# Performance work log

Measured on AMD Instinct MI355X. Metric: run time of the kernel, lower is better.

Reference implementation:

```python
import jax, jax.numpy as jnp
import numpy as np

B, S, D = 512, 500, 128
NQ, NC, NQD, NCD = 10000, 500, 100, 100

def _glorot(key, shape):
    fan_in, fan_out = shape[0], shape[1]
    lim = np.sqrt(6.0 / (fan_in + fan_out))
    return jax.random.uniform(key, shape, jnp.float32, -lim, lim)

def setup_inputs() -> dict:
    key = jax.random.key(0)
    ks = jax.random.split(key, 24)
    inp = {
        'question_seq': jax.random.randint(ks[0], (B, S), 0, NQ),
        'concept_seq': jax.random.randint(ks[1], (B, S), 0, NC),
        'question_diff_seq': jax.random.randint(ks[2], (B, S), 0, NQD),
        'concept_diff_seq': jax.random.randint(ks[3], (B, S), 0, NCD),
        'correct_seq': jax.random.randint(ks[4], (B, S), 0, 2),
        # embedding tables
        'Eq': jax.random.normal(ks[5], (NQ, D), jnp.float32),
        'Ec': jax.random.normal(ks[6], (NC, D), jnp.float32),
        'Eqd': jax.random.normal(ks[7], (NQD, D), jnp.float32),
        'Ecd': jax.random.normal(ks[8], (NCD, D), jnp.float32),
        'Ecorr': jax.random.normal(ks[9], (2, D), jnp.float32),
        # linear layers (stored as [in, out], y = x @ W + b)
        'Wx': _glorot(ks[10], (4 * D, D)), 'bx': jnp.zeros((D,), jnp.float32),
        'Wsdf1': _glorot(ks[11], (D, D)), 'bsdf1': jnp.zeros((D,), jnp.float32),
        'Wsdf2': _glorot(ks[12], (D, D)), 'bsdf2': jnp.zeros((D,), jnp.float32),
        'Wpka1': _glorot(ks[13], (2 * D, D)), 'bpka1': jnp.zeros((D,), jnp.float32),
        'Wpka2': _glorot(ks[14], (2 * D, D)), 'bpka2': jnp.zeros((D,), jnp.float32),
        'Wki': _glorot(ks[15], (4 * D, D)), 'bki': jnp.zeros((D,), jnp.float32),
        # xavier_uniform init of h_pre (torch nn.init.xavier_uniform_ on zeros(B, D))
        'h0': _glorot(ks[16], (B, D)),
    }
    return inp

def reference(question_seq, concept_seq, question_diff_seq, concept_diff_seq,
              correct_seq, Eq, Ec, Eqd, Ecd, Ecorr, Wx, bx,
              Wsdf1, bsdf1, Wsdf2, bsdf2, Wpka1, bpka1, Wpka2, bpka2,
              Wki, bki, h0):
    # embed all sequences: [B, S, D]
    qe = Eq[question_seq]
    ce = Ec[concept_seq]
    qde = Eqd[question_diff_seq]
    cde = Ecd[concept_diff_seq]
    co = Ecorr[correct_seq]
    # x_t = generate_x_MLP(concat(...)) precomputed for all timesteps
    x_all = jnp.concatenate([qe, ce, qde, cde], axis=-1) @ Wx + bx  # [B, S, D]

    # time-major slices for scan over t = 0 .. S-2
    tm = lambda a: jnp.swapaxes(a, 0, 1)  # [S, B, D]
    xs = (tm(x_all)[:-1], tm(x_all)[1:], tm(co)[:-1], tm(qde)[:-1], tm(cde)[:-1])

    def step(h_pre, inputs):
        x_t, x_next, co_t, qd_t, cd_t = inputs
        input_sdf = x_t - h_pre
        sdf = jax.nn.sigmoid(input_sdf @ Wsdf1 + bsdf1) * jnp.tanh(input_sdf @ Wsdf2 + bsdf2)
        input_pka = jnp.concatenate([sdf, co_t], axis=-1)
        pka = jax.nn.sigmoid(input_pka @ Wpka1 + bpka1) * jnp.tanh(input_pka @ Wpka2 + bpka2)
        input_ki = jnp.concatenate([h_pre, co_t, qd_t, cd_t], axis=-1)
        gamma = jax.nn.sigmoid(input_ki @ Wki + bki)
        h = gamma * h_pre + (1.0 - gamma) * pka
        y_t = jax.nn.sigmoid(jnp.sum(x_next * h, axis=-1))  # [B]
        return h, y_t

    _, ys = jax.lax.scan(step, h0, xs)  # ys: [S-1, B]
    # y[:, S-1] is never written in the original (stays 0)
    y = jnp.concatenate([ys.T, jnp.zeros((question_seq.shape[0], 1), jnp.float32)], axis=1)
    return y
```

## Files before the change

### kernel.cpp

```cpp
#include <hip/hip_runtime.h>
#include <hip/hip_bf16.h>
#include <cstdint>
#include <cstddef>

#define BB 512
#define SS 500
#define TT 499
#define NRB 256
#define L2E 1.4426950408889634f

typedef float  f32x4  __attribute__((ext_vector_type(4)));
typedef short  bf16x8 __attribute__((ext_vector_type(8)));

#define MFMA16(A, B, C) __builtin_amdgcn_mfma_f32_16x16x32_bf16((A), (B), (C), 0, 0, 0)

static constexpr size_t OFF_TQ    = 0;
static constexpr size_t OFF_TC    = 10240000;
static constexpr size_t OFF_TQD   = 10752000;
static constexpr size_t OFF_TCD   = 10854400;
static constexpr size_t OFF_TCOK  = 10956800;
static constexpr size_t OFF_TP1   = 10957824;
static constexpr size_t OFF_TP2   = 10958848;
static constexpr size_t OFF_TMPA  = 10959872;
static constexpr size_t OFF_TMPB  = 11011072;
static constexpr size_t OFF_WFRAG = 11062272;
static constexpr size_t TOTAL_WS  = 11226112;

__device__ unsigned char g_fb[TOTAL_WS];

__device__ __forceinline__ unsigned short f2bf(float f) {
    union { float f; uint32_t u; } v; v.f = f;
    uint32_t u = v.u;
    uint32_t r = u + 0x7FFFu + ((u >> 16) & 1u);
    return (unsigned short)(r >> 16);
}
__device__ __forceinline__ float fsig(float z) {
    return __builtin_amdgcn_rcpf(1.0f + __expf(-z));
}
__device__ __forceinline__ uint32_t cvtpk(float lo, float hi) {
    uint32_t r;
    asm("v_cvt_pk_bf16_f32 %0, %1, %2" : "=v"(r) : "v"(lo), "v"(hi));
    return r;
}
__device__ __forceinline__ void bar_lgkm() {
    asm volatile("s_waitcnt lgkmcnt(0)" ::: "memory");
    __builtin_amdgcn_s_barrier();
}
__device__ __forceinline__ float sum16(float x) {
    int a = __float_as_int(x);
    int b = __builtin_amdgcn_update_dpp(a, a, 0xB1, 0xF, 0xF, false);
    float s = x + __int_as_float(b);
    int c = __float_as_int(s);
    int d = __builtin_amdgcn_update_dpp(c, c, 0x4E, 0xF, 0xF, false);
    s += __int_as_float(d);
    int e = __float_as_int(s);
    int f = __builtin_amdgcn_update_dpp(e, e, 0x141, 0xF, 0xF, false);
    s += __int_as_float(f);
    int gg = __float_as_int(s);
    int hh = __builtin_amdgcn_update_dpp(gg, gg, 0x140, 0xF, 0xF, false);
    return s + __int_as_float(hh);
}

__global__ __launch_bounds__(128) void k_tables(
    const float* __restrict__ Eq, const float* __restrict__ Ec,
    const float* __restrict__ Eqd, const float* __restrict__ Ecd,
    const float* __restrict__ Ecorr,
    const float* __restrict__ Wx,  const float* __restrict__ bx,
    const float* __restrict__ Wpka1, const float* __restrict__ bpka1,
    const float* __restrict__ Wpka2, const float* __restrict__ bpka2,
    const float* __restrict__ Wki, const float* __restrict__ bki,
    float* __restrict__ TQ, float* __restrict__ TC,
    float* __restrict__ TQD, float* __restrict__ TCD,
    float* __restrict__ TCOk, float* __restrict__ Tp1, float* __restrict__ Tp2,
    float* __restrict__ tmpA, float* __restrict__ tmpB)
{
    int blk = blockIdx.x;
    const float* A; const float* W; const float* bias = nullptr; float* out; int row;
    int ostride = 1;
    float oscale = 1.0f;
    if      (blk < 10000) { A = Eq;    row = blk;          W = Wx;              bias = bx;    out = TQ;   ostride = 2; }
    else if (blk < 10500) { A = Ec;    row = blk - 10000;  W = Wx  + 128*128;                 out = TC;   ostride = 2; }
    else if (blk < 10600) { A = Eqd;   row = blk - 10500;  W = Wx  + 256*128;                 out = TQD;  ostride = 2; }
    else if (blk < 10700) { A = Ecd;   row = blk - 10600;  W = Wx  + 384*128;                 out = TCD;  ostride = 2; }
    else if (blk < 10800) { A = Eqd;   row = blk - 10700;  W = Wki + 256*128;                 out = tmpA; }
    else if (blk < 10900) { A = Ecd;   row = blk - 10800;  W = Wki + 384*128;                 out = tmpB; }
    else if (blk < 10902) { A = Ecorr; row = blk - 10900;  W = Wki + 128*128;   bias = bki;   out = TCOk; oscale = -L2E; }
    else if (blk < 10904) { A = Ecorr; row = blk - 10902;  W = Wpka1 + 128*128; bias = bpka1; out = Tp1;  oscale = -L2E; }
    else                  { A = Ecorr; row = blk - 10904;  W = Wpka2 + 128*128; bias = bpka2; out = Tp2;  oscale = -2.0f*L2E; }

    __shared__ float a[128];
    int c = threadIdx.x;
    a[c] = A[row * 128 + c];
    __syncthreads();
    float acc = bias ? bias[c] : 0.0f;
    #pragma unroll 8
    for (int k = 0; k < 128; ++k) acc += a[k] * W[k * 128 + c];
    out[(size_t)(row * 128 + c) * ostride] = acc * oscale;
}

__global__ __launch_bounds__(128) void k_tables2(
    const float* __restrict__ Wki,
    float* __restrict__ TQ, float* __restrict__ TC,
    float* __restrict__ TQD, float* __restrict__ TCD,
    const float* __restrict__ tmpA, const float* __restrict__ tmpB)
{
    int blk = blockIdx.x;
    float* base2; const float* tmp = nullptr; int row;
    if      (blk < 10000) { row = blk;          base2 = TQ  + (size_t)row * 256; }
    else if (blk < 10500) { row = blk - 10000;  base2 = TC  + (size_t)row * 256; }
    else if (blk < 10600) { row = blk - 10500;  base2 = TQD + (size_t)row * 256; tmp = tmpA + (size_t)row * 128; }
    else                  { row = blk - 10600;  base2 = TCD + (size_t)row * 256; tmp = tmpB + (size_t)row * 128; }
    __shared__ float a[128];
    int c = threadIdx.x;
    a[c] = base2[c * 2];
    __syncthreads();
    float acc = tmp ? tmp[c] : 0.0f;
    #pragma unroll 8
    for (int k = 0; k < 128; ++k) acc += a[k] * Wki[k * 128 + c];
    base2[c * 2 + 1] = acc * (-L2E);
}

__global__ __launch_bounds__(64) void k_wfrag(
    const float* __restrict__ Wsdf1, const float* __restrict__ Wsdf2,
    const float* __restrict__ Wpka1, const float* __restrict__ Wpka2,
    const float* __restrict__ Wki, unsigned short* __restrict__ wfrag)
{
    int bid = blockIdx.x;
    int m = bid >> 5, w = (bid >> 2) & 7, kt = bid & 3;
    const float* W = (m == 0) ? Wsdf1 : (m == 1) ? Wsdf2 : (m == 2) ? Wpka1 : (m == 3) ? Wpka2 : Wki;
    float sgn = (m == 0) ? -L2E : (m == 1) ? -2.0f*L2E : (m == 2) ? -L2E : (m == 3) ? -2.0f*L2E : L2E;
    int l = threadIdx.x;
    int cc = w * 16 + (l & 15);
    int k0 = kt * 32 + ((l >> 4) << 3);
    unsigned short v[8];
    #pragma unroll
    for (int j = 0; j < 8; ++j) v[j] = f2bf(sgn * W[(size_t)(k0 + j) * 128 + cc]);
    unsigned short* dst = wfrag + ((( (size_t)m * 8 + w) * 4 + kt) * 64 + l) * 8;
    #pragma unroll
    for (int j = 0; j < 8; ++j) dst[j] = v[j];
}

__global__ __launch_bounds__(512, 2) void k_rec(
    const int* __restrict__ qs, const int* __restrict__ cs,
    const int* __restrict__ qds, const int* __restrict__ cds, const int* __restrict__ corr,
    const float2* __restrict__ TQ, const float2* __restrict__ TC,
    const float2* __restrict__ TQD, const float2* __restrict__ TCD,
    const float* __restrict__ TCOk,
    const unsigned short* __restrict__ wfrag,
    const float* __restrict__ Tp1, const float* __restrict__ Tp2,
    const float* __restrict__ bsdf1, const float* __restrict__ bsdf2,
    const float* __restrict__ h0, float* __restrict__ y)
{
    int rb = blockIdx.x;
    int tid = threadIdx.x;
    int w = tid >> 6, l = tid & 63;
    int g = l >> 4, cl = l & 15;
    int col = w * 16 + cl;
    int row = g & 1;
    bool owner = (g < 2);

    __shared__ __align__(16) unsigned short dbuf[256];
    __shared__ __align__(16) unsigned short sbuf[256];
    __shared__ __align__(16) float ybuf[2][2][8];

    bf16x8 wf[5][4];
    #pragma unroll
    for (int m = 0; m < 5; ++m)
        #pragma unroll
        for (int kt = 0; kt < 4; ++kt)
            wf[m][kt] = *(const bf16x8*)(wfrag + ((((size_t)m * 8 + w) * 4 + kt) * 64 + l) * 8);

    float bs1 = bsdf1[col] * (-L2E);
    float bs2 = bsdf2[col] * (-2.0f * L2E);
    float tp1a = Tp1[col], tp1b = Tp1[128 + col];
    float tp2a = Tp2[col], tp2b = Tp2[128 + col];

    float h = h0[(size_t)(rb * 2 + row) * 128 + col];

    char* pdw = (char*)dbuf + row * 256 + ((col * 2) ^ (row << 6));
    char* psw = (char*)sbuf + row * 256 + ((col * 2) ^ (row << 6));
    const bf16x8* prd[4]; const bf16x8* prs[4];
    int rrow = cl & 1;
    #pragma unroll
    for (int kt = 0; kt < 4; ++kt) {
        int off = rrow * 256 + ((kt * 64 + g * 16) ^ (rrow << 6));
        prd[kt] = (const bf16x8*)((char*)dbuf + off);
        prs[kt] = (const bf16x8*)((char*)sbuf + off);
    }

    int boff = (rb * 2 + row) * SS;
    float* yrow = y + (size_t)(rb * 2) * SS;

    float kip_c, x_c_unused; unsigned int c_c;
    {
        int iq = qs[boff], ic = cs[boff], iqd = qds[boff], icd = cds[boff], ico = corr[boff];
        float2 q = TQ[(size_t)iq * 128 + col], c_ = TC[(size_t)ic * 128 + col];
        float2 qd = TQD[(size_t)iqd * 128 + col], cd = TCD[(size_t)icd * 128 + col];
        float co = TCOk[(size_t)ico * 128 + col];
        float x0 = q.x + c_.x + qd.x + cd.x;
        kip_c = q.y + c_.y + qd.y + cd.y + co;
        c_c = (unsigned int)ico & 1u;
        uint32_t pk = cvtpk(x0 - h, x0 - h);
        if (owner) *(unsigned short*)pdw = (unsigned short)pk;
    }
    bar_lgkm();

    #pragma unroll 2
    for (int t = 0; t < TT; ++t) {
        int op = boff + t + 1;
        int iq = qs[op], ic = cs[op], iqd = qds[op], icd = cds[op], ico = corr[op];
        float2 gq = TQ[(size_t)iq * 128 + col], gc = TC[(size_t)ic * 128 + col];
        float2 gqd = TQD[(size_t)iqd * 128 + col], gcd = TCD[(size_t)icd * 128 + col];
        float gco = TCOk[(size_t)ico * 128 + col];

        f32x4 s1a = {bs1, bs1, bs1, bs1}, s1b = {0.f, 0.f, 0.f, 0.f};
        f32x4 s2a = {bs2, bs2, bs2, bs2}, s2b = {0.f, 0.f, 0.f, 0.f};
        f32x4 gda = {0.f, 0.f, 0.f, 0.f}, gdb = {0.f, 0.f, 0.f, 0.f};
        {
            bf16x8 d0 = *prd[0], d1 = *prd[1], d2 = *prd[2], d3 = *prd[3];
            s1a = MFMA16(d0, wf[0][0], s1a); s2a = MFMA16(d0, wf[1][0], s2a); gda = MFMA16(d0, wf[4][0], gda);
            s1b = MFMA16(d2, wf[0][2], s1b); s2b = MFMA16(d2, wf[1][2], s2b); gdb = MFMA16(d2, wf[4][2], gdb);
            s1a = MFMA16(d1, wf[0][1], s1a); s2a = MFMA16(d1, wf[1][1], s2a); gda = MFMA16(d1, wf[4][1], gda);
            s1b = MFMA16(d3, wf[0][3], s1b); s2b = MFMA16(d3, wf[1][3], s2b); gdb = MFMA16(d3, wf[4][3], gdb);
        }
        float s1v = (row ? s1a[1] : s1a[0]) + (row ? s1b[1] : s1b[0]);
        float s2v = (row ? s2a[1] : s2a[0]) + (row ? s2b[1] : s2b[0]);
        float gdv = (row ? gda[1] : gda[0]) + (row ? gdb[1] : gdb[0]);
        float gv = __builtin_amdgcn_rcpf(1.0f + __builtin_amdgcn_exp2f(gdv + kip_c));
        float e1 = __builtin_amdgcn_exp2f(s1v), e2 = __builtin_amdgcn_exp2f(s2v);
        float sdf = (1.0f - e2) * __builtin_amdgcn_rcpf((1.0f + e1) * (1.0f + e2));
        {
            uint32_t pk = cvtpk(sdf, sdf);
            if (owner) *(unsigned short*)psw = (unsigned short)pk;
        }
        bar_lgkm();

        if (t > 0 && w == 0 && l < 2) {
            const float* yb = ybuf[(t - 1) & 1][l];
            float s = (yb[0] + yb[1]) + (yb[2] + yb[3]) + (yb[4] + yb[5]) + (yb[6] + yb[7]);
            yrow[(size_t)l * SS + (t - 1)] = fsig(s);
        }

        f32x4 p1a = {0.f, 0.f, 0.f, 0.f}, p1b = {0.f, 0.f, 0.f, 0.f};
        f32x4 p2a = {0.f, 0.f, 0.f, 0.f}, p2b = {0.f, 0.f, 0.f, 0.f};
        {
            bf16x8 f0 = *prs[0], f1 = *prs[1], f2 = *prs[2], f3 = *prs[3];
            p1a = MFMA16(f0, wf[2][0], p1a); p2a = MFMA16(f0, wf[3][0], p2a);
            p1b = MFMA16(f2, wf[2][2], p1b); p2b = MFMA16(f2, wf[3][2], p2b);
            p1a = MFMA16(f1, wf[2][1], p1a); p2a = MFMA16(f1, wf[3][1], p2a);
            p1b = MFMA16(f3, wf[2][3], p1b); p2b = MFMA16(f3, wf[3][3], p2b);
        }
        float p1v = (row ? p1a[1] : p1a[0]) + (row ? p1b[1] : p1b[0]);
        float p2v = (row ? p2a[1] : p2a[0]) + (row ? p2b[1] : p2b[0]);
        float t1 = c_c ? tp1b : tp1a;
        float t2 = c_c ? tp2b : tp2a;
        float e1p = __builtin_amdgcn_exp2f(p1v + t1), e2p = __builtin_amdgcn_exp2f(p2v + t2);
        float pka = (1.0f - e2p) * __builtin_amdgcn_rcpf((1.0f + e1p) * (1.0f + e2p));
        h = gv * (h - pka) + pka;

        float xn = gq.x + gc.x + gqd.x + gcd.x;
        {
            uint32_t pk = cvtpk(xn - h, xn - h);
            if (owner) *(unsigned short*)pdw = (unsigned short)pk;
        }
        float yv = sum16(xn * h);
        if (owner && cl == 0) ybuf[t & 1][row][w] = yv;
        bar_lgkm();

        kip_c = gq.y + gc.y + gqd.y + gcd.y + gco;
        c_c = (unsigned int)ico & 1u;
    }

    if (w == 0 && l < 2) {
        const float* yb = ybuf[(TT - 1) & 1][l];
        float s = (yb[0] + yb[1]) + (yb[2] + yb[3]) + (yb[4] + yb[5]) + (yb[6] + yb[7]);
        yrow[(size_t)l * SS + (TT - 1)] = fsig(s);
        yrow[(size_t)l * SS + TT] = 0.0f;
    }
}

extern "C" void kernel_launch(void* const* d_in, const int* in_sizes, int n_in,
                              void* d_out, int out_size, void* d_ws, size_t ws_size,
                              hipStream_t stream) {
    const int* qs    = (const int*)d_in[0];
    const int* cs    = (const int*)d_in[1];
    const int* qds   = (const int*)d_in[2];
    const int* cds   = (const int*)d_in[3];
    const int* corr  = (const int*)d_in[4];
    const float* Eq    = (const float*)d_in[5];
    const float* Ec    = (const float*)d_in[6];
    const float* Eqd   = (const float*)d_in[7];
    const float* Ecd   = (const float*)d_in[8];
    const float* Ecorr = (const float*)d_in[9];
    const float* Wx    = (const float*)d_in[10];
    const float* bx    = (const float*)d_in[11];
    const float* Wsdf1 = (const float*)d_in[12];
    const float* bsdf1 = (const float*)d_in[13];
    const float* Wsdf2 = (const float*)d_in[14];
    const float* bsdf2 = (const float*)d_in[15];
    const float* Wpka1 = (const float*)d_in[16];
    const float* bpka1 = (const float*)d_in[17];
    const float* Wpka2 = (const float*)d_in[18];
    const float* bpka2 = (const float*)d_in[19];
    const float* Wki   = (const float*)d_in[20];
    const float* bki   = (const float*)d_in[21];
    const float* h0    = (const float*)d_in[22];

    char* base;
    if (ws_size >= TOTAL_WS) {
        base = (char*)d_ws;
    } else {
        void* p = nullptr;
        hipGetSymbolAddress(&p, HIP_SYMBOL(g_fb));
        base = (char*)p;
    }

    float* TQ    = (float*)(base + OFF_TQ);
    float* TC    = (float*)(base + OFF_TC);
    float* TQD   = (float*)(base + OFF_TQD);
    float* TCD   = (float*)(base + OFF_TCD);
    float* TCOk  = (float*)(base + OFF_TCOK);
    float* Tp1   = (float*)(base + OFF_TP1);
    float* Tp2   = (float*)(base + OFF_TP2);
    float* tmpA  = (float*)(base + OFF_TMPA);
    float* tmpB  = (float*)(base + OFF_TMPB);
    unsigned short* wfrag = (unsigned short*)(base + OFF_WFRAG);

    k_tables<<<10906, 128, 0, stream>>>(Eq, Ec, Eqd, Ecd, Ecorr, Wx, bx,
                                        Wpka1, bpka1, Wpka2, bpka2, Wki, bki,
                                        TQ, TC, TQD, TCD, TCOk, Tp1, Tp2, tmpA, tmpB);
    k_tables2<<<10700, 128, 0, stream>>>(Wki, TQ, TC, TQD, TCD, tmpA, tmpB);
    k_wfrag<<<160, 64, 0, stream>>>(Wsdf1, Wsdf2, Wpka1, Wpka2, Wki, wfrag);
    k_rec<<<NRB, 512, 0, stream>>>(qs, cs, qds, cds, corr,
                                   (const float2*)TQ, (const float2*)TC,
                                   (const float2*)TQD, (const float2*)TCD, TCOk,
                                   wfrag, Tp1, Tp2, bsdf1, bsdf2, h0, (float*)d_out);
}
```

Before: 527.5 us.

## Pre-gather per-step embeddings into packed bf16 time-major stream before recurrence

Adds a fully parallel gather kernel that, for every timestep, looks up the four embedding tables and sums them into a packed bf16 pair (x and the gate contribution), stored time-major, plus a packed byte of the correctness bits. The recurrent kernel then loads one coalesced 32-bit word per step instead of five index loads and five dependent table gathers, taking that latency off the serial critical path. The gate term is also folded into the MFMA accumulator initialisation. The cost is an extra pass writing and reading about 130 MB of workspace, plus bf16 rounding of x and of the gate input.

New measurement: 502.4 us. -4.8%, faster.

```diff
diff --git a/kernel.cpp b/kernel.cpp
--- a/kernel.cpp
+++ b/kernel.cpp
@@ -24,7 +24,9 @@
 static constexpr size_t OFF_TMPA  = 10959872;
 static constexpr size_t OFF_TMPB  = 11011072;
 static constexpr size_t OFF_WFRAG = 11062272;
-static constexpr size_t TOTAL_WS  = 11226112;
+static constexpr size_t OFF_CPK   = 11226112;
+static constexpr size_t OFF_STRM  = 11357184;
+static constexpr size_t TOTAL_WS  = 142429184;
 
 __device__ unsigned char g_fb[TOTAL_WS];
 
@@ -37,6 +39,8 @@
 __device__ __forceinline__ float fsig(float z) {
     return __builtin_amdgcn_rcpf(1.0f + __expf(-z));
 }
+__device__ __forceinline__ float upk_x(uint32_t p) { return __uint_as_float(p & 0xffff0000u); }
+__device__ __forceinline__ float upk_k(uint32_t p) { return __uint_as_float(p << 16); }
 __device__ __forceinline__ uint32_t cvtpk(float lo, float hi) {
     uint32_t r;
     asm("v_cvt_pk_bf16_f32 %0, %1, %2" : "=v"(r) : "v"(lo), "v"(hi));
@@ -140,12 +144,46 @@
     for (int j = 0; j < 8; ++j) dst[j] = v[j];
 }
 
-__global__ __launch_bounds__(512, 2) void k_rec(
+__global__ __launch_bounds__(512) void k_gather(
     const int* __restrict__ qs, const int* __restrict__ cs,
     const int* __restrict__ qds, const int* __restrict__ cds, const int* __restrict__ corr,
     const float2* __restrict__ TQ, const float2* __restrict__ TC,
     const float2* __restrict__ TQD, const float2* __restrict__ TCD,
     const float* __restrict__ TCOk,
+    uint32_t* __restrict__ strm, unsigned char* __restrict__ cpk)
+{
+    int bid = blockIdx.x;
+    int t = bid >> 7, chunk = bid & 127;
+    int tid = threadIdx.x;
+    int b = chunk * 4 + (tid >> 7);
+    int col = tid & 127;
+
+    int iq  = qs  [(size_t)b * SS + t];
+    int ic  = cs  [(size_t)b * SS + t];
+    int iqd = qds [(size_t)b * SS + t];
+    int icd = cds [(size_t)b * SS + t];
+    int ico = corr[(size_t)b * SS + t];
+
+    float2 q  = TQ [(size_t)iq  * 128 + col];
+    float2 c_ = TC [(size_t)ic  * 128 + col];
+    float2 qd = TQD[(size_t)iqd * 128 + col];
+    float2 cd = TCD[(size_t)icd * 128 + col];
+    float  co = TCOk[(size_t)ico * 128 + col];
+
+    float xs = q.x + c_.x + qd.x + cd.x;
+    float ks = q.y + c_.y + qd.y + cd.y + co;
+    strm[((size_t)t * BB + b) * 128 + col] = cvtpk(ks, xs);
+
+    if (tid < 2) {
+        int rb = chunk * 2 + tid;
+        unsigned char bpk = (unsigned char)((corr[(size_t)(rb * 2) * SS + t] & 1)
+                          | ((corr[(size_t)(rb * 2 + 1) * SS + t] & 1) << 1));
+        cpk[(size_t)rb * 512 + t] = bpk;
+    }
+}
+
+__global__ __launch_bounds__(512, 2) void k_rec(
+    const uint32_t* __restrict__ strm, const unsigned char* __restrict__ cpkg,
     const unsigned short* __restrict__ wfrag,
     const float* __restrict__ Tp1, const float* __restrict__ Tp2,
     const float* __restrict__ bsdf1, const float* __restrict__ bsdf2,
@@ -188,18 +226,18 @@
         prs[kt] = (const bf16x8*)((char*)sbuf + off);
     }
 
-    int boff = (rb * 2 + row) * SS;
+    const size_t TSTR = (size_t)BB * 128;
+    const uint32_t* sp = strm + (size_t)(rb * 2 + row) * 128 + col;
+    const unsigned char* cp = cpkg + (size_t)rb * 512;
+
     float* yrow = y + (size_t)(rb * 2) * SS;
 
-    float kip_c, x_c_unused; unsigned int c_c;
+    float kip_c; unsigned int c_c;
     {
-        int iq = qs[boff], ic = cs[boff], iqd = qds[boff], icd = cds[boff], ico = corr[boff];
-        float2 q = TQ[(size_t)iq * 128 + col], c_ = TC[(size_t)ic * 128 + col];
-        float2 qd = TQD[(size_t)iqd * 128 + col], cd = TCD[(size_t)icd * 128 + col];
-        float co = TCOk[(size_t)ico * 128 + col];
-        float x0 = q.x + c_.x + qd.x + cd.x;
-        kip_c = q.y + c_.y + qd.y + cd.y + co;
-        c_c = (unsigned int)ico & 1u;
+        uint32_t p0 = sp[0];
+        kip_c = upk_k(p0);
+        c_c = (cp[0] >> row) & 1u;
+        float x0 = upk_x(p0);
         uint32_t pk = cvtpk(x0 - h, x0 - h);
         if (owner) *(unsigned short*)pdw = (unsigned short)pk;
     }
@@ -207,15 +245,12 @@
 
     #pragma unroll 2
     for (int t = 0; t < TT; ++t) {
-        int op = boff + t + 1;
-        int iq = qs[op], ic = cs[op], iqd = qds[op], icd = cds[op], ico = corr[op];
-        float2 gq = TQ[(size_t)iq * 128 + col], gc = TC[(size_t)ic * 128 + col];
-        float2 gqd = TQD[(size_t)iqd * 128 + col], gcd = TCD[(size_t)icd * 128 + col];
-        float gco = TCOk[(size_t)ico * 128 + col];
+        uint32_t pkN = sp[(size_t)(t + 1) * TSTR];
+        unsigned char cN = cp[t + 1];
 
         f32x4 s1a = {bs1, bs1, bs1, bs1}, s1b = {0.f, 0.f, 0.f, 0.f};
         f32x4 s2a = {bs2, bs2, bs2, bs2}, s2b = {0.f, 0.f, 0.f, 0.f};
-        f32x4 gda = {0.f, 0.f, 0.f, 0.f}, gdb = {0.f, 0.f, 0.f, 0.f};
+        f32x4 gda = {kip_c, kip_c, kip_c, kip_c}, gdb = {0.f, 0.f, 0.f, 0.f};
         {
             bf16x8 d0 = *prd[0], d1 = *prd[1], d2 = *prd[2], d3 = *prd[3];
             s1a = MFMA16(d0, wf[0][0], s1a); s2a = MFMA16(d0, wf[1][0], s2a); gda = MFMA16(d0, wf[4][0], gda);
@@ -226,7 +261,7 @@
         float s1v = (row ? s1a[1] : s1a[0]) + (row ? s1b[1] : s1b[0]);
         float s2v = (row ? s2a[1] : s2a[0]) + (row ? s2b[1] : s2b[0]);
         float gdv = (row ? gda[1] : gda[0]) + (row ? gdb[1] : gdb[0]);
-        float gv = __builtin_amdgcn_rcpf(1.0f + __builtin_amdgcn_exp2f(gdv + kip_c));
+        float gv = __builtin_amdgcn_rcpf(1.0f + __builtin_amdgcn_exp2f(gdv));
         float e1 = __builtin_amdgcn_exp2f(s1v), e2 = __builtin_amdgcn_exp2f(s2v);
         float sdf = (1.0f - e2) * __builtin_amdgcn_rcpf((1.0f + e1) * (1.0f + e2));
         {
@@ -258,7 +293,7 @@
         float pka = (1.0f - e2p) * __builtin_amdgcn_rcpf((1.0f + e1p) * (1.0f + e2p));
         h = gv * (h - pka) + pka;
 
-        float xn = gq.x + gc.x + gqd.x + gcd.x;
+        float xn = upk_x(pkN);
         {
             uint32_t pk = cvtpk(xn - h, xn - h);
             if (owner) *(unsigned short*)pdw = (unsigned short)pk;
@@ -267,8 +302,8 @@
         if (owner && cl == 0) ybuf[t & 1][row][w] = yv;
         bar_lgkm();
 
-        kip_c = gq.y + gc.y + gqd.y + gcd.y + gco;
-        c_c = (unsigned int)ico & 1u;
+        kip_c = upk_k(pkN);
+        c_c = ((unsigned int)cN >> row) & 1u;
     }
 
     if (w == 0 && l < 2) {
@@ -325,14 +360,18 @@
     float* tmpA  = (float*)(base + OFF_TMPA);
     float* tmpB  = (float*)(base + OFF_TMPB);
     unsigned short* wfrag = (unsigned short*)(base + OFF_WFRAG);
+    unsigned char*  cpk   = (unsigned char*)(base + OFF_CPK);
+    uint32_t* strm = (uint32_t*)(base + OFF_STRM);
 
     k_tables<<<10906, 128, 0, stream>>>(Eq, Ec, Eqd, Ecd, Ecorr, Wx, bx,
                                         Wpka1, bpka1, Wpka2, bpka2, Wki, bki,
                                         TQ, TC, TQD, TCD, TCOk, Tp1, Tp2, tmpA, tmpB);
     k_tables2<<<10700, 128, 0, stream>>>(Wki, TQ, TC, TQD, TCD, tmpA, tmpB);
     k_wfrag<<<160, 64, 0, stream>>>(Wsdf1, Wsdf2, Wpka1, Wpka2, Wki, wfrag);
-    k_rec<<<NRB, 512, 0, stream>>>(qs, cs, qds, cds, corr,
-                                   (const float2*)TQ, (const float2*)TC,
-                                   (const float2*)TQD, (const float2*)TCD, TCOk,
-                                   wfrag, Tp1, Tp2, bsdf1, bsdf2, h0, (float*)d_out);
-}
+    k_gather<<<SS * 128, 512, 0, stream>>>(qs, cs, qds, cds, corr,
+                                           (const float2*)TQ, (const float2*)TC,
+                                           (const float2*)TQD, (const float2*)TCD, TCOk,
+                                           strm, cpk);
+    k_rec<<<NRB, 512, 0, stream>>>(strm, cpk, wfrag, Tp1, Tp2,
+                                   bsdf1, bsdf2, h0, (float*)d_out);
+}
```
